# Performance work log

Hardware: AMD Instinct MI355X
Metric: run time of the kernel (lower is better)

The kernel has to match this reference:

```python
import jax, jax.numpy as jnp
import numpy as np

N_NODES = 10000
N_EDGES = 320000
D = 256
D_OUT = 256
NUM_REL = 2


def setup_inputs() -> dict:
    key = jax.random.key(0)
    ks = jax.random.split(key, 16)
    s = 1.0 / np.sqrt(D)
    inp = {}
    inp['feat'] = jax.random.normal(ks[0], (N_NODES, D), dtype=jnp.float32)
    inp['src'] = jax.random.randint(ks[1], (N_EDGES,), 0, N_NODES, dtype=jnp.int32)
    inp['dst'] = jax.random.randint(ks[2], (N_EDGES,), 0, N_NODES, dtype=jnp.int32)
    inp['rel'] = jax.random.randint(ks[3], (N_EDGES,), 0, NUM_REL, dtype=jnp.int32)
    # per-relation edgeNN: ONE tied Linear(D, D) applied twice with relu
    inp['W_rel'] = jax.random.normal(ks[4], (NUM_REL, D, D), dtype=jnp.float32) * s
    inp['b_rel'] = jax.random.normal(ks[5], (NUM_REL, D), dtype=jnp.float32) * s
    # LSTM (single step from zero state: W_hh contributes 0, omitted)
    inp['W_ih'] = jax.random.normal(ks[6], (4 * D, D), dtype=jnp.float32) * s
    inp['b_ih'] = jax.random.normal(ks[7], (4 * D,), dtype=jnp.float32) * s
    inp['b_hh'] = jax.random.normal(ks[8], (4 * D,), dtype=jnp.float32) * s
    # global_update MLP: D -> D/2 -> D/2 -> D_OUT
    h = D // 2
    inp['W1'] = jax.random.normal(ks[9], (h, D), dtype=jnp.float32) * s
    inp['b1'] = jax.random.normal(ks[10], (h,), dtype=jnp.float32) * s
    inp['W2'] = jax.random.normal(ks[11], (h, h), dtype=jnp.float32) * (1.0 / np.sqrt(h))
    inp['b2'] = jax.random.normal(ks[12], (h,), dtype=jnp.float32) * (1.0 / np.sqrt(h))
    inp['W3'] = jax.random.normal(ks[13], (D_OUT, h), dtype=jnp.float32) * (1.0 / np.sqrt(h))
    inp['b3'] = jax.random.normal(ks[14], (D_OUT,), dtype=jnp.float32) * (1.0 / np.sqrt(h))
    return inp


def reference(feat, src, dst, rel, W_rel, b_rel, W_ih, b_ih, b_hh,
              W1, b1, W2, b2, W3, b3):
    n_nodes = feat.shape[0]
    # ---- message: per-edge relation-typed tied-weight MLP ----
    S = feat[src]  # [E, D] gather of source features

    def edge_nn(x, W, b):
        h = jax.nn.relu(x @ W.T + b)
        return jax.nn.relu(h @ W.T + b)  # same lin1 applied twice (tied)

    msgs = jnp.zeros_like(S)
    for r in range(W_rel.shape[0]):  # small fixed relation count
        msgs = jnp.where((rel == r)[:, None], edge_nn(S, W_rel[r], b_rel[r]), msgs)

    # ---- reduce: scatter-sum into destination nodes ----
    agg = jax.ops.segment_sum(msgs, dst, num_segments=n_nodes)  # [N, D]

    # ---- apply: per-node single-step LSTM from zero (h0, c0) ----
    gates = agg @ W_ih.T + b_ih + b_hh  # [N, 4D], torch gate order i,f,g,o
    i, f, g, o = jnp.split(gates, 4, axis=-1)
    c = jax.nn.sigmoid(i) * jnp.tanh(g)  # f * c0 = 0
    hn = jax.nn.sigmoid(o) * jnp.tanh(c)  # [N, D]

    # ---- global_update MLP ----
    x = jax.nn.relu(hn @ W1.T + b1)
    x = jax.nn.relu(x @ W2.T + b2)
    return x @ W3.T + b3  # [N, D_OUT]
```

## Files before the change

kernel.cpp:

```cpp
#include <hip/hip_runtime.h>
#include <hip/hip_bf16.h>

#define N_NODES 10000
#define N_EDGES 320000
#define D 256

typedef __attribute__((ext_vector_type(8))) _Float16 f16x8;
typedef __attribute__((ext_vector_type(4))) _Float16 f16x4;
typedef __attribute__((ext_vector_type(4))) float f32x4;

__device__ __forceinline__ void async_copy16(const void* g, void* l) {
  __builtin_amdgcn_global_load_lds(
      (const __attribute__((address_space(1))) unsigned int*)g,
      (__attribute__((address_space(3))) unsigned int*)l, 16, 0, 0);
}

template<int ROWS, int WAVES>
__device__ __forceinline__ void stage_tile(const _Float16* __restrict__ Wb, int k0, int K,
                                           _Float16* Bs, int wave, int lane) {
  const int sr = lane >> 2, ss = lane & 3;
#pragma unroll
  for (int grp = wave; grp < ROWS / 16; grp += WAVES) {
    int r = grp * 16 + sr;
    int gq = ss ^ ((r >> 1) & 3);
    async_copy16(Wb + (size_t)r * K + k0 + gq * 8, Bs + grp * 512);
  }
}
__device__ __forceinline__ f16x8 read_B(const _Float16* Bs, int r, int quad) {
  return *(const f16x8*)(Bs + r * 32 + (quad ^ ((r >> 1) & 3)) * 8);
}

__device__ __forceinline__ float fast_sigmoid(float x) {
  return __builtin_amdgcn_rcpf(1.f + __expf(-x));
}
__device__ __forceinline__ float fast_tanh(float x) {
  float ax = fabsf(x);
  float e = __expf(-2.f * ax);
  float t = (1.f - e) * __builtin_amdgcn_rcpf(1.f + e);
  return copysignf(t, x);
}

__global__ __launch_bounds__(512) void prep_cast(
    int* __restrict__ cnt,
    const float* __restrict__ W_rel, const float* __restrict__ W_ih,
    const float* __restrict__ b_ih, const float* __restrict__ b_hh,
    const float* __restrict__ W1, const float* __restrict__ W2,
    const float* __restrict__ W3,
    _Float16* __restrict__ W_relh, _Float16* __restrict__ Wg,
    float* __restrict__ bg,
    _Float16* __restrict__ W1h, _Float16* __restrict__ W2h,
    _Float16* __restrict__ W3h) {
  int i = blockIdx.x * 512 + threadIdx.x;
  if (i < 10240) { if (i < N_NODES) cnt[i] = 0; return; }
  i -= 10240;
  if (i < 131072) { W_relh[i] = (_Float16)W_rel[i]; return; }
  i -= 131072;
  if (i < 196608) {
    int p = i >> 8, k = i & 255;
    int t = p / 48, rem = p - t * 48;
    int phase = rem >> 4, u = rem & 15;
    int orig = t * 16 + u + (phase == 1 ? 512 : (phase == 2 ? 768 : 0));
    Wg[i] = (_Float16)W_ih[orig * 256 + k]; return;
  }
  i -= 196608;
  if (i < 32768) { W1h[i] = (_Float16)W1[i]; return; }
  i -= 32768;
  if (i < 16384) { W2h[i] = (_Float16)W2[i]; return; }
  i -= 16384;
  if (i < 32768) { W3h[i] = (_Float16)W3[i]; return; }
  i -= 32768;
  if (i < 768) {
    int t = i / 48, rem = i - t * 48;
    int phase = rem >> 4, u = rem & 15;
    int orig = t * 16 + u + (phase == 1 ? 512 : (phase == 2 ? 768 : 0));
    bg[i] = b_ih[orig] + b_hh[orig];
  }
}

__global__ __launch_bounds__(512) void edge_fill(
    const float* __restrict__ feat, const _Float16* __restrict__ W_relh,
    const float* __restrict__ b_rel, _Float16* __restrict__ Mh,
    const int* __restrict__ dst, const int* __restrict__ src,
    const int* __restrict__ rel,
    int* __restrict__ cnt, unsigned int* __restrict__ rowoff)
{
  __shared__ _Float16 Hs[64 * 266];
  __shared__ alignas(16) _Float16 Bs[256 * 32];
  const int b = blockIdx.x;
  if (b >= 314) {
    int i = (b - 314) * 512 + threadIdx.x;
    int v = dst[i];
    int pos = atomicAdd(&cnt[v], 1);
    if (pos < 128)
      rowoff[(v << 7) + pos] = (unsigned int)((rel[i] * N_NODES + src[i]) * D);
    return;
  }
  const int t = threadIdx.x;
  const int wave = t >> 6, lane = t & 63;
  const int quad = lane >> 4, lrow = lane & 15;
  const int z = (b >= 157) ? 1 : 0;
  const int m0 = (b - z * 157) * 64;
  const _Float16* Wb = W_relh + z * 65536;
  const float* bb = b_rel + z * 256;
  const int wm = (wave >> 2) * 32;
  const int wn = (wave & 3) * 64;

  int ar0 = m0 + wm + lrow;      if (ar0 > N_NODES - 1) ar0 = N_NODES - 1;
  int ar1 = m0 + wm + 16 + lrow; if (ar1 > N_NODES - 1) ar1 = N_NODES - 1;
  const float* fr0 = feat + (size_t)ar0 * 256;
  const float* fr1 = feat + (size_t)ar1 * 256;

  f32x4 acc[2][4];
#pragma unroll
  for (int i = 0; i < 2; ++i)
#pragma unroll
    for (int j = 0; j < 4; ++j) acc[i][j] = (f32x4)0.0f;

#pragma unroll
  for (int kc = 0; kc < 8; ++kc) {
    stage_tile<256, 8>(Wb, kc * 32, 256, Bs, wave, lane);
    float4 u0 = *(const float4*)(fr0 + kc * 32 + quad * 8);
    float4 u1 = *(const float4*)(fr0 + kc * 32 + quad * 8 + 4);
    float4 v0 = *(const float4*)(fr1 + kc * 32 + quad * 8);
    float4 v1 = *(const float4*)(fr1 + kc * 32 + quad * 8 + 4);
    f16x8 af0, af1;
    af0[0] = (_Float16)u0.x; af0[1] = (_Float16)u0.y; af0[2] = (_Float16)u0.z; af0[3] = (_Float16)u0.w;
    af0[4] = (_Float16)u1.x; af0[5] = (_Float16)u1.y; af0[6] = (_Float16)u1.z; af0[7] = (_Float16)u1.w;
    af1[0] = (_Float16)v0.x; af1[1] = (_Float16)v0.y; af1[2] = (_Float16)v0.z; af1[3] = (_Float16)v0.w;
    af1[4] = (_Float16)v1.x; af1[5] = (_Float16)v1.y; af1[6] = (_Float16)v1.z; af1[7] = (_Float16)v1.w;
    __syncthreads();
#pragma unroll
    for (int j = 0; j < 4; ++j) {
      f16x8 bf = read_B(Bs, wn + j * 16 + lrow, quad);
      acc[0][j] = __builtin_amdgcn_mfma_f32_16x16x32_f16(af0, bf, acc[0][j], 0, 0, 0);
      acc[1][j] = __builtin_amdgcn_mfma_f32_16x16x32_f16(af1, bf, acc[1][j], 0, 0, 0);
    }
    __syncthreads();
  }
#pragma unroll
  for (int i = 0; i < 2; ++i) {
    int rb = wm + i * 16 + quad * 4;
#pragma unroll
    for (int j = 0; j < 4; ++j) {
      int col = wn + j * 16 + lrow;
      float bv = bb[col];
#pragma unroll
      for (int reg = 0; reg < 4; ++reg) {
        Hs[(rb + reg) * 266 + col] = (_Float16)fmaxf(acc[i][j][reg] + bv, 0.f);
        acc[i][j][reg] = 0.f;
      }
    }
  }
  __syncthreads();

#pragma unroll
  for (int kc = 0; kc < 8; ++kc) {
    stage_tile<256, 8>(Wb, kc * 32, 256, Bs, wave, lane);
    f16x8 af0 = *(const f16x8*)(Hs + (wm + lrow) * 266 + kc * 32 + quad * 8);
    f16x8 af1 = *(const f16x8*)(Hs + (wm + 16 + lrow) * 266 + kc * 32 + quad * 8);
    __syncthreads();
#pragma unroll
    for (int j = 0; j < 4; ++j) {
      f16x8 bf = read_B(Bs, wn + j * 16 + lrow, quad);
      acc[0][j] = __builtin_amdgcn_mfma_f32_16x16x32_f16(af0, bf, acc[0][j], 0, 0, 0);
      acc[1][j] = __builtin_amdgcn_mfma_f32_16x16x32_f16(af1, bf, acc[1][j], 0, 0, 0);
    }
    __syncthreads();
  }
  _Float16* Mo = Mh + (size_t)z * (N_NODES * D);
#pragma unroll
  for (int i = 0; i < 2; ++i) {
    int rb = m0 + wm + i * 16 + quad * 4;
#pragma unroll
    for (int j = 0; j < 4; ++j) {
      int col = wn + j * 16 + lrow;
      float bv = bb[col];
#pragma unroll
      for (int reg = 0; reg < 4; ++reg) {
        int gm = rb + reg;
        if (gm < N_NODES)
          Mo[(size_t)gm * D + col] = (_Float16)fmaxf(acc[i][j][reg] + bv, 0.f);
      }
    }
  }
}

__global__ __launch_bounds__(256) void agg_kernel(const int* __restrict__ cnt,
                                                  const unsigned int* __restrict__ rowoff,
                                                  const _Float16* __restrict__ Mh,
                                                  _Float16* __restrict__ aggh) {
  __shared__ float part[4][256];
  const int node = blockIdx.x;
  const int wave = threadIdx.x >> 6, lane = threadIdx.x & 63;
  const int base = node << 7;
  const int deg = cnt[node];
  float a0 = 0.f, a1 = 0.f, a2 = 0.f, a3 = 0.f;
  for (int j = wave; j < deg; j += 4) {
    unsigned int off = rowoff[base + j];
    f16x4 v = *(const f16x4*)(Mh + (size_t)off + lane * 4);
    a0 += (float)v[0]; a1 += (float)v[1]; a2 += (float)v[2]; a3 += (float)v[3];
  }
  *(float4*)&part[wave][lane * 4] = make_float4(a0, a1, a2, a3);
  __syncthreads();
  if (wave == 0) {
    float4 p0 = *(const float4*)&part[0][lane * 4];
    float4 p1 = *(const float4*)&part[1][lane * 4];
    float4 p2 = *(const float4*)&part[2][lane * 4];
    float4 p3 = *(const float4*)&part[3][lane * 4];
    f16x4 o;
    o[0] = (_Float16)(p0.x + p1.x + p2.x + p3.x);
    o[1] = (_Float16)(p0.y + p1.y + p2.y + p3.y);
    o[2] = (_Float16)(p0.z + p1.z + p2.z + p3.z);
    o[3] = (_Float16)(p0.w + p1.w + p2.w + p3.w);
    *(f16x4*)(aggh + (size_t)node * D + lane * 4) = o;
  }
}

__global__ __launch_bounds__(256) void tail(
    const _Float16* __restrict__ aggh,
    const _Float16* __restrict__ Wg, const float* __restrict__ bg,
    const _Float16* __restrict__ W1h, const float* __restrict__ b1,
    const _Float16* __restrict__ W2h, const float* __restrict__ b2,
    const _Float16* __restrict__ W3h, const float* __restrict__ b3,
    float* __restrict__ out)
{
  __shared__ alignas(16) _Float16 Ws[768 * 32];
  __shared__ _Float16 Hn[16 * 266];
  __shared__ _Float16 Xs[16 * 138];
  __shared__ _Float16 X2s[16 * 138];
  const int t = threadIdx.x;
  const int wave = t >> 6, lane = t & 63;
  const int quad = lane >> 4, lrow = lane & 15;
  const int r0 = blockIdx.x * 16;

  {
    f16x8 af[8];
#pragma unroll
    for (int kc = 0; kc < 8; ++kc)
      af[kc] = *(const f16x8*)(aggh + (size_t)(r0 + lrow) * 256 + kc * 32 + quad * 8);
    f32x4 acc[12];
#pragma unroll
    for (int j = 0; j < 12; ++j) acc[j] = (f32x4)0.0f;
#pragma unroll
    for (int kc = 0; kc < 8; ++kc) {
      stage_tile<768, 4>(Wg, kc * 32, 256, Ws, wave, lane);
      __syncthreads();
#pragma unroll
      for (int j = 0; j < 12; ++j) {
        f16x8 bf = read_B(Ws, (wave * 12 + j) * 16 + lrow, quad);
        acc[j] = __builtin_amdgcn_mfma_f32_16x16x32_f16(af[kc], bf, acc[j], 0, 0, 0);
      }
      __syncthreads();
    }
#pragma unroll
    for (int p = 0; p < 4; ++p) {
      float bvi = bg[(wave * 12 + 3 * p + 0) * 16 + lrow];
      float bvg = bg[(wave * 12 + 3 * p + 1) * 16 + lrow];
      float bvo = bg[(wave * 12 + 3 * p + 2) * 16 + lrow];
      int dcol = (wave * 4 + p) * 16 + lrow;
#pragma unroll
      for (int reg = 0; reg < 4; ++reg) {
        float vi = acc[3 * p + 0][reg] + bvi;
        float vg = acc[3 * p + 1][reg] + bvg;
        float vo = acc[3 * p + 2][reg] + bvo;
        float c = fast_sigmoid(vi) * fast_tanh(vg);
        Hn[(quad * 4 + reg) * 266 + dcol] = (_Float16)(fast_sigmoid(vo) * fast_tanh(c));
      }
    }
  }
  __syncthreads();

  {
    f16x8 af[8];
#pragma unroll
    for (int kc = 0; kc < 8; ++kc)
      af[kc] = *(const f16x8*)(Hn + lrow * 266 + kc * 32 + quad * 8);
    f32x4 acc[2];
    acc[0] = (f32x4)0.0f; acc[1] = (f32x4)0.0f;
#pragma unroll
    for (int kc = 0; kc < 8; ++kc) {
      stage_tile<128, 4>(W1h, kc * 32, 256, Ws, wave, lane);
      __syncthreads();
#pragma unroll
      for (int j = 0; j < 2; ++j) {
        f16x8 bf = read_B(Ws, wave * 32 + j * 16 + lrow, quad);
        acc[j] = __builtin_amdgcn_mfma_f32_16x16x32_f16(af[kc], bf, acc[j], 0, 0, 0);
      }
      __syncthreads();
    }
#pragma unroll
    for (int j = 0; j < 2; ++j) {
      int col = wave * 32 + j * 16 + lrow;
      float bv = b1[col];
#pragma unroll
      for (int reg = 0; reg < 4; ++reg)
        Xs[(quad * 4 + reg) * 138 + col] = (_Float16)fmaxf(acc[j][reg] + bv, 0.f);
    }
  }
  __syncthreads();

  {
    f16x8 af[4];
#pragma unroll
    for (int kc = 0; kc < 4; ++kc)
      af[kc] = *(const f16x8*)(Xs + lrow * 138 + kc * 32 + quad * 8);
    f32x4 acc[2];
    acc[0] = (f32x4)0.0f; acc[1] = (f32x4)0.0f;
#pragma unroll
    for (int kc = 0; kc < 4; ++kc) {
      stage_tile<128, 4>(W2h, kc * 32, 128, Ws, wave, lane);
      __syncthreads();
#pragma unroll
      for (int j = 0; j < 2; ++j) {
        f16x8 bf = read_B(Ws, wave * 32 + j * 16 + lrow, quad);
        acc[j] = __builtin_amdgcn_mfma_f32_16x16x32_f16(af[kc], bf, acc[j], 0, 0, 0);
      }
      __syncthreads();
    }
#pragma unroll
    for (int j = 0; j < 2; ++j) {
      int col = wave * 32 + j * 16 + lrow;
      float bv = b2[col];
#pragma unroll
      for (int reg = 0; reg < 4; ++reg)
        X2s[(quad * 4 + reg) * 138 + col] = (_Float16)fmaxf(acc[j][reg] + bv, 0.f);
    }
  }
  __syncthreads();

  {
    f16x8 af[4];
#pragma unroll
    for (int kc = 0; kc < 4; ++kc)
      af[kc] = *(const f16x8*)(X2s + lrow * 138 + kc * 32 + quad * 8);
    f32x4 acc[4];
#pragma unroll
    for (int j = 0; j < 4; ++j) acc[j] = (f32x4)0.0f;
#pragma unroll
    for (int kc = 0; kc < 4; ++kc) {
      stage_tile<256, 4>(W3h, kc * 32, 128, Ws, wave, lane);
      __syncthreads();
#pragma unroll
      for (int j = 0; j < 4; ++j) {
        f16x8 bf = read_B(Ws, wave * 64 + j * 16 + lrow, quad);
        acc[j] = __builtin_amdgcn_mfma_f32_16x16x32_f16(af[kc], bf, acc[j], 0, 0, 0);
      }
      __syncthreads();
    }
#pragma unroll
    for (int j = 0; j < 4; ++j) {
      int col = wave * 64 + j * 16 + lrow;
      float bv = b3[col];
#pragma unroll
      for (int reg = 0; reg < 4; ++reg)
        out[(size_t)(r0 + quad * 4 + reg) * 256 + col] = acc[j][reg] + bv;
    }
  }
}

extern "C" void kernel_launch(void* const* d_in, const int* in_sizes, int n_in,
                              void* d_out, int out_size, void* d_ws, size_t ws_size,
                              hipStream_t stream) {
  const float* feat  = (const float*)d_in[0];
  const int* src = (const int*)d_in[1];
  const int* dst = (const int*)d_in[2];
  const int* rel = (const int*)d_in[3];
  const float* W_rel = (const float*)d_in[4];
  const float* b_rel = (const float*)d_in[5];
  const float* W_ih  = (const float*)d_in[6];
  const float* b_ih  = (const float*)d_in[7];
  const float* b_hh  = (const float*)d_in[8];
  const float* W1 = (const float*)d_in[9];
  const float* b1 = (const float*)d_in[10];
  const float* W2 = (const float*)d_in[11];
  const float* b2 = (const float*)d_in[12];
  const float* W3 = (const float*)d_in[13];
  const float* b3 = (const float*)d_in[14];
  float* out = (float*)d_out;

  char* ws = (char*)d_ws;
  _Float16* Mh   = (_Float16*)(ws);
  _Float16* aggh = (_Float16*)(ws + 10240000);
  char* wsb = ws + 15360000;
  _Float16* W_relh = (_Float16*)(wsb);
  _Float16* Wg     = (_Float16*)(wsb + 262144);
  _Float16* W1h    = (_Float16*)(wsb + 655360);
  _Float16* W2h    = (_Float16*)(wsb + 720896);
  _Float16* W3h    = (_Float16*)(wsb + 753664);
  float*    bg     = (float*)(wsb + 819200);
  int*      cnt    = (int*)(wsb + 822272);
  unsigned int* rowoff = (unsigned int*)(wsb + 862272);

  prep_cast<<<822, 512, 0, stream>>>(cnt, W_rel, W_ih, b_ih, b_hh, W1, W2, W3,
                                     W_relh, Wg, bg, W1h, W2h, W3h);
  edge_fill<<<939, 512, 0, stream>>>(feat, W_relh, b_rel, Mh,
                                     dst, src, rel, cnt, rowoff);
  agg_kernel<<<N_NODES, 256, 0, stream>>>(cnt, rowoff, Mh, aggh);
  tail<<<625, 256, 0, stream>>>(aggh, Wg, bg, W1h, b1, W2h, b2, W3h, b3, out);
}
```

Before: 193.8 us.

## Load tail-kernel weights directly from global memory and double waves per block

The tail kernel no longer stages weight tiles into shared memory with async copies and barriers. Each wave now reads its B fragments straight from global memory (served by L2/L1), and the block grows from 4 to 8 waves so each wave owns half as many output columns. This removes the per-k-chunk __syncthreads pairs and frees the 48KB shared buffer, which may raise occupancy. The cost is uncoalesced, uncached-in-LDS weight reads that every block repeats.

```diff
diff --git a/kernel.cpp b/kernel.cpp
--- a/kernel.cpp
+++ b/kernel.cpp
@@ -28,6 +28,11 @@
 }
 __device__ __forceinline__ f16x8 read_B(const _Float16* Bs, int r, int quad) {
   return *(const f16x8*)(Bs + r * 32 + (quad ^ ((r >> 1) & 3)) * 8);
+}
+
+__device__ __forceinline__ f16x8 load_B(const _Float16* __restrict__ W, int row, int K,
+                                        int kc, int quad) {
+  return *(const f16x8*)(W + (size_t)row * K + kc * 32 + quad * 8);
 }
 
 __device__ __forceinline__ float fast_sigmoid(float x) {
@@ -216,7 +221,7 @@
   }
 }
 
-__global__ __launch_bounds__(256) void tail(
+__global__ __launch_bounds__(512) void tail(
     const _Float16* __restrict__ aggh,
     const _Float16* __restrict__ Wg, const float* __restrict__ bg,
     const _Float16* __restrict__ W1h, const float* __restrict__ b1,
@@ -224,7 +229,6 @@
     const _Float16* __restrict__ W3h, const float* __restrict__ b3,
     float* __restrict__ out)
 {
-  __shared__ alignas(16) _Float16 Ws[768 * 32];
   __shared__ _Float16 Hn[16 * 266];
   __shared__ _Float16 Xs[16 * 138];
   __shared__ _Float16 X2s[16 * 138];
@@ -238,26 +242,23 @@
 #pragma unroll
     for (int kc = 0; kc < 8; ++kc)
       af[kc] = *(const f16x8*)(aggh + (size_t)(r0 + lrow) * 256 + kc * 32 + quad * 8);
-    f32x4 acc[12];
-#pragma unroll
-    for (int j = 0; j < 12; ++j) acc[j] = (f32x4)0.0f;
+    f32x4 acc[6];
+#pragma unroll
+    for (int j = 0; j < 6; ++j) acc[j] = (f32x4)0.0f;
 #pragma unroll
     for (int kc = 0; kc < 8; ++kc) {
-      stage_tile<768, 4>(Wg, kc * 32, 256, Ws, wave, lane);
-      __syncthreads();
-#pragma unroll
-      for (int j = 0; j < 12; ++j) {
-        f16x8 bf = read_B(Ws, (wave * 12 + j) * 16 + lrow, quad);
+#pragma unroll
+      for (int j = 0; j < 6; ++j) {
+        f16x8 bf = load_B(Wg, (wave * 6 + j) * 16 + lrow, 256, kc, quad);
         acc[j] = __builtin_amdgcn_mfma_f32_16x16x32_f16(af[kc], bf, acc[j], 0, 0, 0);
       }
-      __syncthreads();
-    }
-#pragma unroll
-    for (int p = 0; p < 4; ++p) {
-      float bvi = bg[(wave * 12 + 3 * p + 0) * 16 + lrow];
-      float bvg = bg[(wave * 12 + 3 * p + 1) * 16 + lrow];
-      float bvo = bg[(wave * 12 + 3 * p + 2) * 16 + lrow];
-      int dcol = (wave * 4 + p) * 16 + lrow;
+    }
+#pragma unroll
+    for (int p = 0; p < 2; ++p) {
+      float bvi = bg[(wave * 6 + 3 * p + 0) * 16 + lrow];
+      float bvg = bg[(wave * 6 + 3 * p + 1) * 16 + lrow];
+      float bvo = bg[(wave * 6 + 3 * p + 2) * 16 + lrow];
+      int dcol = (wave * 2 + p) * 16 + lrow;
 #pragma unroll
       for (int reg = 0; reg < 4; ++reg) {
         float vi = acc[3 * p + 0][reg] + bvi;
@@ -275,81 +276,57 @@
 #pragma unroll
     for (int kc = 0; kc < 8; ++kc)
       af[kc] = *(const f16x8*)(Hn + lrow * 266 + kc * 32 + quad * 8);
+    f32x4 acc = (f32x4)0.0f;
+#pragma unroll
+    for (int kc = 0; kc < 8; ++kc) {
+      f16x8 bf = load_B(W1h, wave * 16 + lrow, 256, kc, quad);
+      acc = __builtin_amdgcn_mfma_f32_16x16x32_f16(af[kc], bf, acc, 0, 0, 0);
+    }
+    int col = wave * 16 + lrow;
+    float bv = b1[col];
+#pragma unroll
+    for (int reg = 0; reg < 4; ++reg)
+      Xs[(quad * 4 + reg) * 138 + col] = (_Float16)fmaxf(acc[reg] + bv, 0.f);
+  }
+  __syncthreads();
+
+  {
+    f16x8 af[4];
+#pragma unroll
+    for (int kc = 0; kc < 4; ++kc)
+      af[kc] = *(const f16x8*)(Xs + lrow * 138 + kc * 32 + quad * 8);
+    f32x4 acc = (f32x4)0.0f;
+#pragma unroll
+    for (int kc = 0; kc < 4; ++kc) {
+      f16x8 bf = load_B(W2h, wave * 16 + lrow, 128, kc, quad);
+      acc = __builtin_amdgcn_mfma_f32_16x16x32_f16(af[kc], bf, acc, 0, 0, 0);
+    }
+    int col = wave * 16 + lrow;
+    float bv = b2[col];
+#pragma unroll
+    for (int reg = 0; reg < 4; ++reg)
+      X2s[(quad * 4 + reg) * 138 + col] = (_Float16)fmaxf(acc[reg] + bv, 0.f);
+  }
+  __syncthreads();
+
+  {
+    f16x8 af[4];
+#pragma unroll
+    for (int kc = 0; kc < 4; ++kc)
+      af[kc] = *(const f16x8*)(X2s + lrow * 138 + kc * 32 + quad * 8);
     f32x4 acc[2];
     acc[0] = (f32x4)0.0f; acc[1] = (f32x4)0.0f;
 #pragma unroll
-    for (int kc = 0; kc < 8; ++kc) {
-      stage_tile<128, 4>(W1h, kc * 32, 256, Ws, wave, lane);
-      __syncthreads();
+    for (int kc = 0; kc < 4; ++kc) {
 #pragma unroll
       for (int j = 0; j < 2; ++j) {
-        f16x8 bf = read_B(Ws, wave * 32 + j * 16 + lrow, quad);
+        f16x8 bf = load_B(W3h, wave * 32 + j * 16 + lrow, 128, kc, quad);
         acc[j] = __builtin_amdgcn_mfma_f32_16x16x32_f16(af[kc], bf, acc[j], 0, 0, 0);
       }
-      __syncthreads();
     }
 #pragma unroll
     for (int j = 0; j < 2; ++j) {
       int col = wave * 32 + j * 16 + lrow;
-      float bv = b1[col];
-#pragma unroll
-      for (int reg = 0; reg < 4; ++reg)
-        Xs[(quad * 4 + reg) * 138 + col] = (_Float16)fmaxf(acc[j][reg] + bv, 0.f);
-    }
-  }
-  __syncthreads();
-
-  {
-    f16x8 af[4];
-#pragma unroll
-    for (int kc = 0; kc < 4; ++kc)
-      af[kc] = *(const f16x8*)(Xs + lrow * 138 + kc * 32 + quad * 8);
-    f32x4 acc[2];
-    acc[0] = (f32x4)0.0f; acc[1] = (f32x4)0.0f;
-#pragma unroll
-    for (int kc = 0; kc < 4; ++kc) {
-      stage_tile<128, 4>(W2h, kc * 32, 128, Ws, wave, lane);
-      __syncthreads();
-#pragma unroll
-      for (int j = 0; j < 2; ++j) {
-        f16x8 bf = read_B(Ws, wave * 32 + j * 16 + lrow, quad);
-        acc[j] = __builtin_amdgcn_mfma_f32_16x16x32_f16(af[kc], bf, acc[j], 0, 0, 0);
-      }
-      __syncthreads();
-    }
-#pragma unroll
-    for (int j = 0; j < 2; ++j) {
-      int col = wave * 32 + j * 16 + lrow;
-      float bv = b2[col];
-#pragma unroll
-      for (int reg = 0; reg < 4; ++reg)
-        X2s[(quad * 4 + reg) * 138 + col] = (_Float16)fmaxf(acc[j][reg] + bv, 0.f);
-    }
-  }
-  __syncthreads();
-
-  {
-    f16x8 af[4];
-#pragma unroll
-    for (int kc = 0; kc < 4; ++kc)
-      af[kc] = *(const f16x8*)(X2s + lrow * 138 + kc * 32 + quad * 8);
-    f32x4 acc[4];
-#pragma unroll
-    for (int j = 0; j < 4; ++j) acc[j] = (f32x4)0.0f;
-#pragma unroll
-    for (int kc = 0; kc < 4; ++kc) {
-      stage_tile<256, 4>(W3h, kc * 32, 128, Ws, wave, lane);
-      __syncthreads();
-#pragma unroll
-      for (int j = 0; j < 4; ++j) {
-        f16x8 bf = read_B(Ws, wave * 64 + j * 16 + lrow, quad);
-        acc[j] = __builtin_amdgcn_mfma_f32_16x16x32_f16(af[kc], bf, acc[j], 0, 0, 0);
-      }
-      __syncthreads();
-    }
-#pragma unroll
-    for (int j = 0; j < 4; ++j) {
-      int col = wave * 64 + j * 16 + lrow;
       float bv = b3[col];
 #pragma unroll
       for (int reg = 0; reg < 4; ++reg)
@@ -396,5 +373,5 @@
   edge_fill<<<939, 512, 0, stream>>>(feat, W_relh, b_rel, Mh,
                                      dst, src, rel, cnt, rowoff);
   agg_kernel<<<N_NODES, 256, 0, stream>>>(cnt, rowoff, Mh, aggh);
-  tail<<<625, 256, 0, stream>>>(aggh, Wg, bg, W1h, b1, W2h, b2, W3h, b3, out);
-}
+  tail<<<625, 512, 0, stream>>>(aggh, Wg, bg, W1h, b1, W2h, b2, W3h, b3, out);
+}
```

Measured after the change: 213.1 us. +10.0%, slower.
